# Performance work log

Measured on AMD Instinct MI355X. Metric: run time of the kernel, lower is better.

Reference implementation:

```python
import jax, jax.numpy as jnp
import numpy as np
from jax import lax

B = 8      # batch size
R = 64     # voxel grid resolution
DN = ('NDHWC', 'DHWIO', 'NDHWC')  # conv dimension numbers


def setup_inputs() -> dict:
    key = jax.random.key(0)
    ks = jax.random.split(key, 8)
    N = 200000
    # coords: (batch, x, y, z). Sparse active voxels.
    b = jax.random.randint(ks[0], (N, 1), 0, B, dtype=jnp.int32)
    xyz = jax.random.randint(ks[1], (N, 3), 0, R, dtype=jnp.int32)
    coords = jnp.concatenate([b, xyz], axis=1)
    feats = jax.random.normal(ks[2], (N, 1), dtype=jnp.float32)
    W1 = jax.random.normal(ks[3], (3, 3, 3, 1, 32), dtype=jnp.float32) * 0.2
    W2 = jax.random.normal(ks[4], (2, 2, 2, 32, 64), dtype=jnp.float32) * 0.1
    W3 = jax.random.normal(ks[5], (2, 2, 2, 64, 128), dtype=jnp.float32) * 0.07
    fc_w = jax.random.normal(ks[6], (128, 256), dtype=jnp.float32) * 0.09
    fc_b = jnp.zeros((256,), dtype=jnp.float32)
    return {"coords": coords, "feats": feats, "W1": W1, "W2": W2,
            "W3": W3, "fc_w": fc_w, "fc_b": fc_b}


def _pool_mask(m):
    # active-site mask after a stride-2 kernel-2 sparse conv: any active input
    # voxel in the 2x2x2 block activates the output site.
    return lax.reduce_window(m, 0.0, lax.max, (1, 2, 2, 2, 1), (1, 2, 2, 2, 1), 'VALID')


def reference(coords, feats, W1, W2, W3, fc_w, fc_b):
    b, x, y, z = coords[:, 0], coords[:, 1], coords[:, 2], coords[:, 3]
    # Densify the sparse tensor (duplicate coords summed for determinism)
    grid = jnp.zeros((B, R, R, R, 1), feats.dtype).at[b, x, y, z].add(feats)
    mask = jnp.zeros((B, R, R, R, 1), feats.dtype).at[b, x, y, z].set(1.0)

    # Conv3d(1,32,k=3,s=1): submanifold -> output coords == input coords (mask)
    h = lax.conv_general_dilated(grid, W1, (1, 1, 1), 'SAME', dimension_numbers=DN)
    h = jax.nn.relu(h) * mask

    # Conv3d(32,64,k=2,s=2): downsample; active iff any active input in block
    h = lax.conv_general_dilated(h, W2, (2, 2, 2), 'VALID', dimension_numbers=DN)
    mask2 = _pool_mask(mask)
    h = jax.nn.relu(h) * mask2

    # Conv3d(64,128,k=2,s=2)
    h = lax.conv_general_dilated(h, W3, (2, 2, 2), 'VALID', dimension_numbers=DN)
    mask3 = _pool_mask(mask2)
    h = jax.nn.relu(h) * mask3

    # GlobalAvgPool over ACTIVE voxels only, per batch
    s = jnp.sum(h, axis=(1, 2, 3))                       # [B,128]
    cnt = jnp.sum(mask3, axis=(1, 2, 3))                 # [B,1]
    pooled = s / jnp.maximum(cnt, 1.0)

    return pooled @ fc_w + fc_b                          # [B,256]
```

## Files before the change

kernel.cpp:

```cpp
#include <hip/hip_runtime.h>
#include <hip/hip_bf16.h>
#include <hip/hip_fp16.h>

typedef __attribute__((ext_vector_type(2))) _Float16 f16x2;
typedef __attribute__((ext_vector_type(8))) _Float16 f16x8;
typedef __attribute__((ext_vector_type(4))) float    f32x4;

#define GRID_ELEMS (8*64*64*64)
#define ZERO_U4    540800

__global__ __launch_bounds__(256) void zero_k(uint4* __restrict__ p)
{
  const unsigned i = blockIdx.x * 256 + threadIdx.x;
  if (i < ZERO_U4) p[i] = (uint4){0u, 0u, 0u, 0u};
}

__global__ __launch_bounds__(256) void scatter_setup_k(
    const int* __restrict__ coords, const float* __restrict__ feats,
    const float* __restrict__ W1, const float* __restrict__ W2, const float* __restrict__ W3,
    __half2* __restrict__ gpk,
    uint4* __restrict__ W1f, uint4* __restrict__ W2f,
    uint4* __restrict__ W3fA, uint4* __restrict__ W3fB, int N)
{
  const int bi = blockIdx.x;
  if (bi < 44) {
    const int i = bi * 256 + threadIdx.x;
    if (i < 2048) {
      const int wid = i >> 9, ks = (i >> 6) & 7, lane = i & 63;
      const int l15 = lane & 15, l4 = lane >> 4, o = wid * 16 + l15;
      f16x8 v;
      #pragma unroll
      for (int j = 0; j < 8; ++j)
        v[j] = (_Float16)W2[ks * 2048 + (l4 * 8 + j) * 64 + o];
      W2f[i] = __builtin_bit_cast(uint4, v);
    } else if (i < 10240) {
      const int e = i - 2048, ab = e >> 12, r = e & 4095;
      const int wid = r >> 10, ks = (r >> 6) & 15, lane = r & 63;
      const int l15 = lane & 15, l4 = lane >> 4, o = wid * 32 + l15 + ab * 16;
      f16x8 v;
      #pragma unroll
      for (int j = 0; j < 8; ++j)
        v[j] = (_Float16)W3[(ks >> 1) * 8192 + ((ks & 1) * 32 + l4 * 8 + j) * 128 + o];
      (ab ? W3fB : W3fA)[r] = __builtin_bit_cast(uint4, v);
    } else if (i < 10368) {
      const int t = i - 10240;
      const int mt = t >> 6, l = t & 63;
      f16x8 v;
      #pragma unroll
      for (int j = 0; j < 8; ++j) {
        const int k = (l >> 4) * 8 + j;
        v[j] = (k < 27) ? (_Float16)W1[k * 32 + mt * 16 + (l & 15)] : (_Float16)0;
      }
      W1f[t] = __builtin_bit_cast(uint4, v);
    }
    return;
  }
  const int i = (bi - 44) * 256 + threadIdx.x;
  if (i >= N) return;
  const int4 c = reinterpret_cast<const int4*>(coords)[i];
  const int idx = ((c.x * 64 + c.y) * 64 + c.z) * 64 + c.w;
  const __half2 v = __halves2half2(__float2half_rn(feats[i]), __float2half_rn(1.0f));
  unsafeAtomicAdd(&gpk[idx], v);
}

__global__ __launch_bounds__(256, 5) void mega_k(
    const unsigned* __restrict__ gpk,
    const uint4* __restrict__ W1f, const uint4* __restrict__ W2f,
    const uint4* __restrict__ W3fA, const uint4* __restrict__ W3fB,
    float* __restrict__ spart, float* __restrict__ cntB)
{
  __shared__ __align__(16) char smem[32368];
  _Float16* const h1f  = (_Float16*)(smem + 11264);
  _Float16* const tile = (_Float16*)(smem + 27648);
  float*    const m2s  = (float*)(smem + 31248);
  float*    const m3s  = (float*)(smem + 31760);
  unsigned char* const lists = (unsigned char*)(smem + 31824);
  int*      const lcnt   = (int*)(smem + 32336);
  unsigned* const m2bits = (unsigned*)(smem + 32352);

  const int tid = threadIdx.x;
  const int bid = blockIdx.x;
  const int b   = bid >> 8;
  const int X2  = (bid >> 5) & 7, Y2 = (bid >> 2) & 7, Zp = bid & 3;
  const int gb  = b << 18;
  const int lane = tid & 63, wid = tid >> 6;
  const int l15 = lane & 15, l4 = lane >> 4;

  if (tid < 4) { lcnt[tid] = 0; m2bits[tid] = 0; }
  __syncthreads();

  {
    const int gx0 = X2 * 8 - 1, gy0 = Y2 * 8 - 1, gz0 = Zp * 16 - 1;
    for (int e = tid; e < 1800; e += 256) {
      const int x = e / 180, r = e - x * 180, y = r / 18, z = r - y * 18;
      const int gx = gx0 + x, gy = gy0 + y, gz = gz0 + z;
      const bool ok = ((unsigned)gx < 64u) & ((unsigned)gy < 64u) & ((unsigned)gz < 64u);
      const unsigned g = ok ? gpk[gb + (gx << 12) + (gy << 6) + gz] : 0u;
      tile[e] = __builtin_bit_cast(_Float16, (unsigned short)(g & 0xffffu));
      const int ix = x - 1, iy = y - 1, iz = z - 1;
      if ((((unsigned)ix < 8u) & ((unsigned)iy < 8u) & ((unsigned)iz < 16u)) &&
          (g >> 16) != 0u) {
        const int li = ((iz >> 3) << 1) | (ix & 1);
        const int slot = atomicAdd(&lcnt[li], 1);
        if (slot < 128)
          lists[li * 128 + slot] =
              (unsigned char)(((ix >> 1) << 6) | (iy << 3) | (iz & 7));
        const int v2 = ((ix >> 1) << 5) | ((iy >> 1) << 3) | (iz >> 1);
        atomicOr(&m2bits[v2 >> 5], 1u << (v2 & 31));
      }
    }
  }

  const uint4 w1a = W1f[lane];
  const uint4 w1b = W1f[64 + lane];
  uint4 w2r[8];
  #pragma unroll
  for (int ks = 0; ks < 8; ++ks) w2r[ks] = W2f[(wid * 8 + ks) * 64 + lane];

  int t_off[8];
  #pragma unroll
  for (int j = 0; j < 8; ++j) {
    const int k = l4 * 8 + j;
    int off = 0;
    if (k < 27) {
      const int tx = k / 9, rr = k - 9 * tx, ty = rr / 3, tz = rr - 3 * ty;
      off = (tx * 180 + ty * 18 + tz) * 2;
    }
    t_off[j] = off;
  }

  __syncthreads();

  if (tid < 128)
    m2s[tid] = ((m2bits[tid >> 5] >> (tid & 31)) & 1u) ? 1.f : 0.f;

  const char* tilec = (const char*)tile;
  uint4 wa[4], wb2[4];

  #pragma unroll
  for (int o = 0; o < 2; ++o) {
    f32x4 acc[4];
    #pragma unroll
    for (int nt = 0; nt < 4; ++nt) acc[nt] = (f32x4){0.f, 0.f, 0.f, 0.f};

    #pragma unroll
    for (int cc = 0; cc < 2; ++cc) {
      {
        uint4* zp = reinterpret_cast<uint4*>((char*)h1f + tid * 64);
        const uint4 z4 = (uint4){0u, 0u, 0u, 0u};
        zp[0] = z4; zp[1] = z4; zp[2] = z4; zp[3] = z4;
      }
      __syncthreads();

      const int lc = lcnt[o * 2 + cc];
      for (int g = wid; g * 16 < lc; g += 4) {
        const int slot = g * 16 + l15;
        const bool valid = slot < lc;
        const int idx = valid ? (int)lists[(o * 2 + cc) * 128 + slot] : 0;
        const int x1 = 2 * (idx >> 6) + cc, y1 = (idx >> 3) & 7, zo = idx & 7;
        const int z1 = o * 8 + zo;
        const int base2 = (x1 * 180 + y1 * 18 + z1) * 2;
        f16x8 bf;
        #pragma unroll
        for (int j = 0; j < 8; ++j)
          bf[j] = *reinterpret_cast<const _Float16*>(tilec + base2 + t_off[j]);
        f32x4 aA = (f32x4){0.f, 0.f, 0.f, 0.f};
        f32x4 aB = (f32x4){0.f, 0.f, 0.f, 0.f};
        aA = __builtin_amdgcn_mfma_f32_16x16x32_f16(__builtin_bit_cast(f16x8, w1a), bf, aA, 0, 0, 0);
        aB = __builtin_amdgcn_mfma_f32_16x16x32_f16(__builtin_bit_cast(f16x8, w1b), bf, aB, 0, 0, 0);

        if (valid) {
          const int p_l = ((y1 & 1) << 1) | (zo & 1);
          const int v2  = ((x1 >> 1) << 4) | ((y1 >> 1) << 2) | (zo >> 1);
          const int fbase = (((v2 >> 4) * 4 + p_l) * 64 + (v2 & 15)) * 8 + (l4 & 1) * 4;
          const int qsel = l4 >> 1;
          uint2 wA, wB;
          {
            const auto c0 = __builtin_amdgcn_cvt_pkrtz(fmaxf(aA[0], 0.f), fmaxf(aA[1], 0.f));
            const auto c1 = __builtin_amdgcn_cvt_pkrtz(fmaxf(aA[2], 0.f), fmaxf(aA[3], 0.f));
            wA.x = __builtin_bit_cast(unsigned, c0);
            wA.y = __builtin_bit_cast(unsigned, c1);
          }
          {
            const auto c0 = __builtin_amdgcn_cvt_pkrtz(fmaxf(aB[0], 0.f), fmaxf(aB[1], 0.f));
            const auto c1 = __builtin_amdgcn_cvt_pkrtz(fmaxf(aB[2], 0.f), fmaxf(aB[3], 0.f));
            wB.x = __builtin_bit_cast(unsigned, c0);
            wB.y = __builtin_bit_cast(unsigned, c1);
          }
          *reinterpret_cast<uint2*>(&h1f[fbase + qsel * 128])       = wA;
          *reinterpret_cast<uint2*>(&h1f[fbase + (2 + qsel) * 128]) = wB;
        }
      }
      __syncthreads();

      if (o == 0 && cc == 0 && tid < 16) {
        const int base = ((tid >> 3) << 6) + (((tid >> 2) & 1) << 4) + ((tid & 3) << 1);
        float m = m2s[base];
        m = fmaxf(m, m2s[base + 1]);  m = fmaxf(m, m2s[base + 8]);
        m = fmaxf(m, m2s[base + 9]);  m = fmaxf(m, m2s[base + 32]);
        m = fmaxf(m, m2s[base + 33]); m = fmaxf(m, m2s[base + 40]);
        m = fmaxf(m, m2s[base + 41]);
        m3s[tid] = m;
      }

      #pragma unroll
      for (int ks = 0; ks < 4; ++ks) {
        const f16x8 af = __builtin_bit_cast(f16x8, w2r[cc * 4 + ks]);
        #pragma unroll
        for (int nt = 0; nt < 4; ++nt) {
          const f16x8 bb = *reinterpret_cast<const f16x8*>(&h1f[((nt * 4 + ks) * 64 + lane) * 8]);
          acc[nt] = __builtin_amdgcn_mfma_f32_16x16x32_f16(af, bb, acc[nt], 0, 0, 0);
        }
      }

      if (o == 1 && cc == 1) {
        #pragma unroll
        for (int j = 0; j < 4; ++j) {
          wa[j]  = W3fA[(wid * 16 + j) * 64 + lane];
          wb2[j] = W3fB[(wid * 16 + j) * 64 + lane];
        }
      }
      __syncthreads();
    }

    _Float16* const h2o = (_Float16*)(smem + o * 11264);
    const int o0 = wid * 16 + l4 * 4;
    #pragma unroll
    for (int nt = 0; nt < 4; ++nt) {
      const int v2l = nt * 16 + l15;
      const float m2v = m2s[((v2l >> 4) << 5) + (((v2l >> 2) & 3) << 3) + o * 4 + (v2l & 3)];
      const unsigned um = (m2v != 0.f) ? 0xffffffffu : 0u;
      const auto p0 = __builtin_amdgcn_cvt_pkrtz(fmaxf(acc[nt][0], 0.f), fmaxf(acc[nt][1], 0.f));
      const auto p1 = __builtin_amdgcn_cvt_pkrtz(fmaxf(acc[nt][2], 0.f), fmaxf(acc[nt][3], 0.f));
      uint2 u;
      u.x = __builtin_bit_cast(unsigned, p0) & um;
      u.y = __builtin_bit_cast(unsigned, p1) & um;
      *reinterpret_cast<uint2*>(&h2o[v2l * 88 + o0]) = u;
    }
  }
  __syncthreads();

  f32x4 c3a = (f32x4){0.f,0.f,0.f,0.f};
  f32x4 c3b = (f32x4){0.f,0.f,0.f,0.f};
  const int v3 = l15;
  const int x3 = v3 >> 3, y3 = (v3 >> 2) & 1, z3 = v3 & 3;
  const int obyte = (z3 >> 1) * 11264;

  #pragma unroll
  for (int kc = 0; kc < 4; ++kc) {
    uint4 na[4], nb[4];
    if (kc < 3) {
      #pragma unroll
      for (int j = 0; j < 4; ++j) {
        na[j] = W3fA[(wid * 16 + (kc + 1) * 4 + j) * 64 + lane];
        nb[j] = W3fB[(wid * 16 + (kc + 1) * 4 + j) * 64 + lane];
      }
    }
    #pragma unroll
    for (int j = 0; j < 4; ++j) {
      const int ks = kc * 4 + j;
      const int p = ks >> 1;
      const int x2 = 2 * x3 + (p >> 2), y2 = 2 * y3 + ((p >> 1) & 1);
      const int z2l = 2 * (z3 & 1) + (p & 1);
      const int v2l = (x2 << 4) | (y2 << 2) | z2l;
      const int c0 = (ks & 1) * 32 + l4 * 8;
      const f16x8 bf = *reinterpret_cast<const f16x8*>(smem + obyte + (v2l * 88 + c0) * 2);
      c3a = __builtin_amdgcn_mfma_f32_16x16x32_f16(__builtin_bit_cast(f16x8, wa[j]),  bf, c3a, 0, 0, 0);
      c3b = __builtin_amdgcn_mfma_f32_16x16x32_f16(__builtin_bit_cast(f16x8, wb2[j]), bf, c3b, 0, 0, 0);
    }
    if (kc < 3) {
      #pragma unroll
      for (int j = 0; j < 4; ++j) { wa[j] = na[j]; wb2[j] = nb[j]; }
    }
  }

  const float m3v = m3s[v3];
  float part[2][4];
  #pragma unroll
  for (int j = 0; j < 4; ++j) {
    part[0][j] = fmaxf(c3a[j], 0.f) * m3v;
    part[1][j] = fmaxf(c3b[j], 0.f) * m3v;
  }
  #pragma unroll
  for (int d = 1; d < 16; d <<= 1) {
    #pragma unroll
    for (int mt = 0; mt < 2; ++mt)
      #pragma unroll
      for (int j = 0; j < 4; ++j)
        part[mt][j] += __shfl_xor(part[mt][j], d, 64);
  }
  if (l15 == 0) {
    const int sb = (b * 64 + (bid & 63)) * 128 + wid * 32;
    #pragma unroll
    for (int mt = 0; mt < 2; ++mt)
      #pragma unroll
      for (int j = 0; j < 4; ++j)
        atomicAdd(&spart[sb + mt * 16 + l4 * 4 + j], part[mt][j]);
  }
  if (tid == 0) {
    float t = 0.f;
    #pragma unroll
    for (int i = 0; i < 16; ++i) t += m3s[i];
    atomicAdd(&cntB[b * 64 + (bid & 63)], t);
  }
}

__global__ __launch_bounds__(256) void reduce_fc_k(
    const float* __restrict__ spart, const float* __restrict__ cntB,
    const float* __restrict__ fc_w, const float* __restrict__ fc_b,
    float* __restrict__ out)
{
  __shared__ float s_t[256];
  __shared__ float s_l[128];
  __shared__ float c_l;
  const int b = blockIdx.x, tid = threadIdx.x;
  const int ch = tid & 127, hf = tid >> 7;
  float a = 0.f;
  #pragma unroll 8
  for (int g = hf * 32; g < hf * 32 + 32; ++g)
    a += spart[(b * 64 + g) * 128 + ch];
  s_t[tid] = a;
  if (tid < 64) {
    float cs = cntB[b * 64 + tid];
    #pragma unroll
    for (int d = 1; d < 64; d <<= 1) cs += __shfl_xor(cs, d, 64);
    if (tid == 0) c_l = cs;
  }
  __syncthreads();
  if (tid < 128) s_l[tid] = s_t[tid] + s_t[tid + 128];
  __syncthreads();
  const float inv = 1.f / fmaxf(c_l, 1.f);
  float o = fc_b[tid];
  #pragma unroll 8
  for (int c = 0; c < 128; ++c) o = fmaf(s_l[c] * inv, fc_w[c * 256 + tid], o);
  out[b * 256 + tid] = o;
}

extern "C" void kernel_launch(void* const* d_in, const int* in_sizes, int n_in,
                              void* d_out, int out_size, void* d_ws, size_t ws_size,
                              hipStream_t stream)
{
  const int*   coords = (const int*)  d_in[0];
  const float* feats  = (const float*)d_in[1];
  const float* W1     = (const float*)d_in[2];
  const float* W2     = (const float*)d_in[3];
  const float* W3     = (const float*)d_in[4];
  const float* fc_w   = (const float*)d_in[5];
  const float* fc_b   = (const float*)d_in[6];
  float* out = (float*)d_out;
  const int N = in_sizes[0] / 4;

  unsigned* gpk   = (unsigned*)d_ws;
  float*    spart = (float*)(gpk + GRID_ELEMS);
  float*    cntB  = spart + 8 * 64 * 128;
  uint4*    W1f   = (uint4*)(cntB + 512);
  uint4*    W2f   = W1f + 128;
  uint4*    W3fA  = W2f + 2048;
  uint4*    W3fB  = W3fA + 4096;

  zero_k<<<(ZERO_U4 + 255) / 256, 256, 0, stream>>>((uint4*)gpk);
  scatter_setup_k<<<44 + (N + 255) / 256, 256, 0, stream>>>(
      coords, feats, W1, W2, W3, (__half2*)gpk, W1f, W2f, W3fA, W3fB, N);
  mega_k<<<2048, 256, 0, stream>>>(gpk, W1f, W2f, W3fA, W3fB, spart, cntB);
  reduce_fc_k<<<8, 256, 0, stream>>>(spart, cntB, fc_w, fc_b, out);
}
```

Baseline: 66.40 us.

## Replace dense voxel grid scatter with per-block binned point lists including halos

Instead of zeroing and atomically scattering into an 8M-element dense half2 grid, the scatter kernel bins each point into per-workgroup region lists, duplicating points that fall in neighbouring halos. Each mega_k block then accumulates its tile in fp32 shared memory and builds its active-voxel lists and masks from bitmaps. This removes the large grid memset and the dense halo gather, leaving only a small buffer to zero. In exchange it adds global atomics on per-region counters and relies on a fixed list capacity per region.

```diff
diff --git a/kernel.cpp b/kernel.cpp
--- a/kernel.cpp
+++ b/kernel.cpp
@@ -6,8 +6,9 @@
 typedef __attribute__((ext_vector_type(8))) _Float16 f16x8;
 typedef __attribute__((ext_vector_type(4))) float    f32x4;
 
-#define GRID_ELEMS (8*64*64*64)
-#define ZERO_U4    540800
+#define NREG    2048
+#define RCAP    320
+#define ZERO_U4 17024
 
 __global__ __launch_bounds__(256) void zero_k(uint4* __restrict__ p)
 {
@@ -18,7 +19,7 @@
 __global__ __launch_bounds__(256) void scatter_setup_k(
     const int* __restrict__ coords, const float* __restrict__ feats,
     const float* __restrict__ W1, const float* __restrict__ W2, const float* __restrict__ W3,
-    __half2* __restrict__ gpk,
+    unsigned* __restrict__ rcnt, uint2* __restrict__ rlist,
     uint4* __restrict__ W1f, uint4* __restrict__ W2f,
     uint4* __restrict__ W3fA, uint4* __restrict__ W3fB, int N)
 {
@@ -58,57 +59,65 @@
   const int i = (bi - 44) * 256 + threadIdx.x;
   if (i >= N) return;
   const int4 c = reinterpret_cast<const int4*>(coords)[i];
-  const int idx = ((c.x * 64 + c.y) * 64 + c.z) * 64 + c.w;
-  const __half2 v = __halves2half2(__float2half_rn(feats[i]), __float2half_rn(1.0f));
-  unsafeAtomicAdd(&gpk[idx], v);
+  const float f = feats[i];
+  const int x = c.y, y = c.z, z = c.w;
+
+  int rxs[2], lxs[2], nxc = 1;
+  rxs[0] = x >> 3; lxs[0] = (x & 7) + 1;
+  if ((x & 7) == 0 && rxs[0] > 0)      { rxs[1] = rxs[0] - 1; lxs[1] = 9;  nxc = 2; }
+  else if ((x & 7) == 7 && rxs[0] < 7) { rxs[1] = rxs[0] + 1; lxs[1] = 0;  nxc = 2; }
+  int rys[2], lys[2], nyc = 1;
+  rys[0] = y >> 3; lys[0] = (y & 7) + 1;
+  if ((y & 7) == 0 && rys[0] > 0)      { rys[1] = rys[0] - 1; lys[1] = 9;  nyc = 2; }
+  else if ((y & 7) == 7 && rys[0] < 7) { rys[1] = rys[0] + 1; lys[1] = 0;  nyc = 2; }
+  int rzs[2], lzs[2], nzc = 1;
+  rzs[0] = z >> 4; lzs[0] = (z & 15) + 1;
+  if ((z & 15) == 0 && rzs[0] > 0)       { rzs[1] = rzs[0] - 1; lzs[1] = 17; nzc = 2; }
+  else if ((z & 15) == 15 && rzs[0] < 3) { rzs[1] = rzs[0] + 1; lzs[1] = 0;  nzc = 2; }
+
+  const unsigned fbits = __float_as_uint(f);
+  for (int ax = 0; ax < nxc; ++ax)
+    for (int ay = 0; ay < nyc; ++ay)
+      for (int az = 0; az < nzc; ++az) {
+        const int rid = (c.x << 8) | (rxs[ax] << 5) | (rys[ay] << 2) | rzs[az];
+        const unsigned ta = (unsigned)(lxs[ax] * 180 + lys[ay] * 18 + lzs[az]);
+        unsigned info = 0;
+        if ((ax | ay | az) == 0)
+          info = 0x400u | ((unsigned)(x & 7) << 7) | ((unsigned)(y & 7) << 4)
+                        | (unsigned)(z & 15);
+        const unsigned slot = atomicAdd(&rcnt[rid], 1u);
+        if (slot < RCAP)
+          rlist[(size_t)rid * RCAP + slot] = make_uint2(ta | (info << 16), fbits);
+      }
 }
 
 __global__ __launch_bounds__(256, 5) void mega_k(
-    const unsigned* __restrict__ gpk,
+    const unsigned* __restrict__ rcnt, const uint2* __restrict__ rlist,
     const uint4* __restrict__ W1f, const uint4* __restrict__ W2f,
     const uint4* __restrict__ W3fA, const uint4* __restrict__ W3fB,
     float* __restrict__ spart, float* __restrict__ cntB)
 {
-  __shared__ __align__(16) char smem[32368];
+  __shared__ __align__(16) char smem[32480];
+  float*    const tile32 = (float*)smem;
   _Float16* const h1f  = (_Float16*)(smem + 11264);
   _Float16* const tile = (_Float16*)(smem + 27648);
   float*    const m2s  = (float*)(smem + 31248);
   float*    const m3s  = (float*)(smem + 31760);
   unsigned char* const lists = (unsigned char*)(smem + 31824);
   int*      const lcnt   = (int*)(smem + 32336);
-  unsigned* const m2bits = (unsigned*)(smem + 32352);
+  unsigned* const m1bits = (unsigned*)(smem + 32352);
 
   const int tid = threadIdx.x;
   const int bid = blockIdx.x;
   const int b   = bid >> 8;
-  const int X2  = (bid >> 5) & 7, Y2 = (bid >> 2) & 7, Zp = bid & 3;
-  const int gb  = b << 18;
   const int lane = tid & 63, wid = tid >> 6;
   const int l15 = lane & 15, l4 = lane >> 4;
 
-  if (tid < 4) { lcnt[tid] = 0; m2bits[tid] = 0; }
-  __syncthreads();
-
   {
-    const int gx0 = X2 * 8 - 1, gy0 = Y2 * 8 - 1, gz0 = Zp * 16 - 1;
-    for (int e = tid; e < 1800; e += 256) {
-      const int x = e / 180, r = e - x * 180, y = r / 18, z = r - y * 18;
-      const int gx = gx0 + x, gy = gy0 + y, gz = gz0 + z;
-      const bool ok = ((unsigned)gx < 64u) & ((unsigned)gy < 64u) & ((unsigned)gz < 64u);
-      const unsigned g = ok ? gpk[gb + (gx << 12) + (gy << 6) + gz] : 0u;
-      tile[e] = __builtin_bit_cast(_Float16, (unsigned short)(g & 0xffffu));
-      const int ix = x - 1, iy = y - 1, iz = z - 1;
-      if ((((unsigned)ix < 8u) & ((unsigned)iy < 8u) & ((unsigned)iz < 16u)) &&
-          (g >> 16) != 0u) {
-        const int li = ((iz >> 3) << 1) | (ix & 1);
-        const int slot = atomicAdd(&lcnt[li], 1);
-        if (slot < 128)
-          lists[li * 128 + slot] =
-              (unsigned char)(((ix >> 1) << 6) | (iy << 3) | (iz & 7));
-        const int v2 = ((ix >> 1) << 5) | ((iy >> 1) << 3) | (iz >> 1);
-        atomicOr(&m2bits[v2 >> 5], 1u << (v2 & 31));
-      }
-    }
+    uint4* zp = reinterpret_cast<uint4*>(tile32);
+    for (int e = tid; e < 450; e += 256) zp[e] = (uint4){0u, 0u, 0u, 0u};
+    if (tid < 32) m1bits[tid] = 0;
+    if (tid < 4)  lcnt[tid] = 0;
   }
 
   const uint4 w1a = W1f[lane];
@@ -116,6 +125,44 @@
   uint4 w2r[8];
   #pragma unroll
   for (int ks = 0; ks < 8; ++ks) w2r[ks] = W2f[(wid * 8 + ks) * 64 + lane];
+
+  __syncthreads();
+
+  {
+    int cnt0 = (int)rcnt[bid];
+    if (cnt0 > RCAP) cnt0 = RCAP;
+    for (int e = tid; e < cnt0; e += 256) {
+      const uint2 en = rlist[(size_t)bid * RCAP + e];
+      const int ta = en.x & 0xffffu;
+      const unsigned info = en.x >> 16;
+      atomicAdd(&tile32[ta], __uint_as_float(en.y));
+      if (info & 0x400u) {
+        const int bi2 = info & 0x3ff;
+        const unsigned bit = 1u << (bi2 & 31);
+        const unsigned old = atomicOr(&m1bits[bi2 >> 5], bit);
+        if (!(old & bit)) {
+          const int ix = bi2 >> 7, iy = (bi2 >> 4) & 7, iz = bi2 & 15;
+          const int li = ((iz >> 3) << 1) | (ix & 1);
+          const int slot = atomicAdd(&lcnt[li], 1);
+          lists[li * 128 + slot] =
+              (unsigned char)(((ix >> 1) << 6) | (iy << 3) | (iz & 7));
+        }
+      }
+    }
+  }
+  __syncthreads();
+
+  for (int e = tid; e < 900; e += 256) {
+    const float2 v = *reinterpret_cast<const float2*>(&tile32[e * 2]);
+    const auto pk = __builtin_amdgcn_cvt_pkrtz(v.x, v.y);
+    reinterpret_cast<unsigned*>(tile)[e] = __builtin_bit_cast(unsigned, pk);
+  }
+  if (tid < 128) {
+    const int x2 = tid >> 5, y2 = (tid >> 3) & 3, z2 = tid & 7;
+    const unsigned w0 = m1bits[((2 * x2) << 2) | y2];
+    const unsigned w1 = m1bits[((2 * x2 + 1) << 2) | y2];
+    m2s[tid] = ((w0 | w1) & (0x30003u << (2 * z2))) ? 1.f : 0.f;
+  }
 
   int t_off[8];
   #pragma unroll
@@ -128,11 +175,6 @@
     }
     t_off[j] = off;
   }
-
-  __syncthreads();
-
-  if (tid < 128)
-    m2s[tid] = ((m2bits[tid >> 5] >> (tid & 31)) & 1u) ? 1.f : 0.f;
 
   const char* tilec = (const char*)tile;
   uint4 wa[4], wb2[4];
@@ -350,17 +392,18 @@
   float* out = (float*)d_out;
   const int N = in_sizes[0] / 4;
 
-  unsigned* gpk   = (unsigned*)d_ws;
-  float*    spart = (float*)(gpk + GRID_ELEMS);
+  unsigned* rcnt  = (unsigned*)d_ws;
+  float*    spart = (float*)(rcnt + NREG);
   float*    cntB  = spart + 8 * 64 * 128;
-  uint4*    W1f   = (uint4*)(cntB + 512);
+  uint2*    rlist = (uint2*)(cntB + 512);
+  uint4*    W1f   = (uint4*)(rlist + (size_t)NREG * RCAP);
   uint4*    W2f   = W1f + 128;
   uint4*    W3fA  = W2f + 2048;
   uint4*    W3fB  = W3fA + 4096;
 
-  zero_k<<<(ZERO_U4 + 255) / 256, 256, 0, stream>>>((uint4*)gpk);
+  zero_k<<<(ZERO_U4 + 255) / 256, 256, 0, stream>>>((uint4*)rcnt);
   scatter_setup_k<<<44 + (N + 255) / 256, 256, 0, stream>>>(
-      coords, feats, W1, W2, W3, (__half2*)gpk, W1f, W2f, W3fA, W3fB, N);
-  mega_k<<<2048, 256, 0, stream>>>(gpk, W1f, W2f, W3fA, W3fB, spart, cntB);
+      coords, feats, W1, W2, W3, rcnt, rlist, W1f, W2f, W3fA, W3fB, N);
+  mega_k<<<NREG, 256, 0, stream>>>(rcnt, rlist, W1f, W2f, W3fA, W3fB, spart, cntB);
   reduce_fc_k<<<8, 256, 0, stream>>>(spart, cntB, fc_w, fc_b, out);
 }
```

New measurement: 99.98 us. +50.6%, slower.
